# Kernel tuning notes

Hardware: AMD Instinct MI355X
Metric: run time of the kernel (lower is better)

The kernel has to match this reference:

```python
import jax, jax.numpy as jnp
import numpy as np

TAG_THR = 0.1
MIN_HEIGHT = 0.0
PULL_WEIGHT = 1.0
PUSH_WEIGHT = 1.0
EPS = 1e-6


def _bbox_iou(boxes):
    # boxes: [N,4] -> IoU [N,N] (standard, no +1 offset; heights in the loss
    # are also computed without +1)
    x1, y1, x2, y2 = boxes[:, 0], boxes[:, 1], boxes[:, 2], boxes[:, 3]
    area = (x2 - x1) * (y2 - y1)
    iw = jnp.clip(jnp.minimum(x2[:, None], x2[None, :]) - jnp.maximum(x1[:, None], x1[None, :]), 0.0)
    ih = jnp.clip(jnp.minimum(y2[:, None], y2[None, :]) - jnp.maximum(y1[:, None], y1[None, :]), 0.0)
    inter = iw * ih
    union = area[:, None] + area[None, :] - inter
    return inter / jnp.maximum(union, 1e-12)


def _single_image(pred, gt_inds, proposals):
    # pred [N,D], gt_inds [N] int, proposals [N,5]
    N = pred.shape[0]
    heights = proposals[:, 3] - proposals[:, 1]
    valid = (gt_inds >= 0) & (heights > MIN_HEIGHT)
    scores = proposals[:, 4]
    iou = _bbox_iou(proposals[:, :4])  # [N,N]

    def step(state, _):
        alive, tot_pull, tot_push, pull_cnt, push_cnt = state
        active = jnp.sum(alive) >= 2  # pop i; if nothing remains, the torch loop breaks
        # i = highest-scoring remaining proposal (greedy, score-sorted)
        i = jnp.argmax(jnp.where(alive, scores, -jnp.inf))
        rem = alive.at[i].set(False)
        overlap = (iou[i] > 0.0) & rem
        diff = jnp.mean((pred - pred[i]) ** 2, axis=1)  # [N]
        check = diff < TAG_THR
        same = gt_inds == gt_inds[i]
        pull_m = overlap & same & ~check
        push_m = overlap & ~same & check
        pn = jnp.sum(pull_m)
        qn = jnp.sum(push_m)
        pull_l = jnp.sum(jnp.where(pull_m, diff * scores, 0.0)) / jnp.maximum(pn, 1).astype(diff.dtype)
        push_l = jnp.sum(jnp.where(push_m, jnp.exp(-diff) * scores, 0.0)) / jnp.maximum(qn, 1).astype(diff.dtype)
        add_pull = active & (pn > 0)
        add_push = active & (qn > 0)
        tot_pull = tot_pull + jnp.where(add_pull, pull_l, 0.0)
        tot_push = tot_push + jnp.where(add_push, push_l, 0.0)
        pull_cnt = pull_cnt + add_pull.astype(jnp.float32)
        push_cnt = push_cnt + add_push.astype(jnp.float32)
        # suppress everything overlapping i whose tag is already close (diff < thr)
        new_alive = rem & ~(overlap & check)
        alive = jnp.where(active, new_alive, alive)
        return (alive, tot_pull, tot_push, pull_cnt, push_cnt), None

    z = jnp.float32(0.0)
    init = (valid, z, z, z, z)
    (_, tot_pull, tot_push, pull_cnt, push_cnt), _ = jax.lax.scan(step, init, None, length=N)
    pull = tot_pull / (pull_cnt + EPS)
    push = tot_push / (push_cnt + EPS)
    return push, pull


def setup_inputs() -> dict:
    key = jax.random.key(0)
    k1, k2, k3, k4, k5, k6, k7 = jax.random.split(key, 7)
    IMGS, N, D = 4, 2000, 4
    pred = jax.random.normal(k1, (IMGS, N, D), dtype=jnp.float32)
    gt_inds = jax.random.randint(k2, (IMGS, N), 0, 50, dtype=jnp.int32)
    x1 = jax.random.uniform(k3, (IMGS, N), minval=0.0, maxval=800.0)
    y1 = jax.random.uniform(k4, (IMGS, N), minval=0.0, maxval=800.0)
    w = jax.random.uniform(k5, (IMGS, N), minval=8.0, maxval=128.0)
    h = jax.random.uniform(k6, (IMGS, N), minval=8.0, maxval=128.0)
    score = jax.random.uniform(k7, (IMGS, N), minval=0.0, maxval=1.0)
    proposals = jnp.stack([x1, y1, x1 + w, y1 + h, score], axis=-1).astype(jnp.float32)
    gt_bboxes = jax.random.uniform(jax.random.fold_in(key, 9), (IMGS, 20, 4), dtype=jnp.float32)
    return {"pred": pred, "gt_inds": gt_inds, "proposals": proposals, "gt_bboxes": gt_bboxes}


def reference(pred, gt_inds, proposals, gt_bboxes):
    # gt_bboxes is accepted by the torch forward but never used in the loss math.
    push, pull = jax.vmap(_single_image)(pred, gt_inds, proposals)  # per-image scalars
    img_num = pred.shape[0]
    push_loss = jnp.sum(push) / img_num * PUSH_WEIGHT
    pull_loss = jnp.sum(pull) / img_num * PULL_WEIGHT
    return push_loss, pull_loss
```

## Files before the change

### kernel.cpp

```cpp
#include <hip/hip_runtime.h>
#include <stdint.h>

#define BLOCK 256
#define KMAX 8
#define NWAVES (BLOCK / 64)
#define S2 2048
#define NW 32
#define NCH 32
#define SPB 16
#define PB (S2 / SPB)
#define RB (S2 / BLOCK)
#define PCAP 65536
#define LDSP2 4096
#define BCAP 64
#define EFF_INF 0x7FFFFFFF

__device__ inline int rank_of(const unsigned long long* ss, int j) {
    int jw = j >> 6, jb = j & 63;
    int rk = __popcll(ss[jw] & (jb ? (~0ull >> (64 - jb)) : 0ull));
    for (int w = 0; w < jw; ++w) rk += __popcll(ss[w]);
    return rk;
}

__global__ __launch_bounds__(BLOCK) void rankcount_kernel(
    const float* __restrict__ proposals,
    int* __restrict__ partial, int* __restrict__ pcnt, int N, int imgs)
{
    const int bi = blockIdx.x, bj = blockIdx.y, img = blockIdx.z;
    const int t = threadIdx.x;
    if (bi == 0 && bj == 0 && t == 0) pcnt[img] = 0;
    const float* P = proposals + (size_t)img * N * 5;
    __shared__ unsigned sj[BLOCK];
    const int jbase = bj * BLOCK;
    {
        int j = jbase + t;
        sj[t] = (j < N) ? __float_as_uint(P[j*5 + 4]) : 0u;
    }
    __syncthreads();
    const int i = bi * BLOCK + t;
    if (i >= N) return;
    const unsigned my = __float_as_uint(P[i*5 + 4]);
    int p = 0;
    const uint4* s4 = (const uint4*)sj;
#pragma unroll
    for (int q = 0; q < BLOCK/4; ++q) {
        uint4 v = s4[q];
        int jj = jbase + q*4;
        p += (int)((v.x > my) | ((v.x == my) & (jj + 0 < i)));
        p += (int)((v.y > my) | ((v.y == my) & (jj + 1 < i)));
        p += (int)((v.z > my) | ((v.z == my) & (jj + 2 < i)));
        p += (int)((v.w > my) | ((v.w == my) & (jj + 3 < i)));
    }
    partial[((size_t)(img*RB + bj))*S2 + i] = p;
}

__global__ __launch_bounds__(BLOCK) void rankscatter_kernel(
    const float* __restrict__ pred, const int* __restrict__ gt_inds,
    const float* __restrict__ proposals, const int* __restrict__ partial,
    float* __restrict__ soa, int* __restrict__ sgt, int N, int imgs)
{
    const int img = blockIdx.y, t = threadIdx.x;
    const int i = blockIdx.x * BLOCK + t;
    const size_t stride = (size_t)imgs * S2;
    const size_t base   = (size_t)img * S2;

    if (i >= N) {
        if (i < S2) {
#pragma unroll
            for (int a = 0; a < 9; ++a) soa[(size_t)a*stride + base + i] = 0.f;
            sgt[base + i] = -1;
        }
        return;
    }

    const float* P = proposals + (size_t)img * N * 5;
    const float* E = pred      + (size_t)img * N * 4;
    const int*   G = gt_inds   + (size_t)img * N;

    const float p0 = P[i*5+0], p1 = P[i*5+1], p2 = P[i*5+2],
                p3 = P[i*5+3], p4 = P[i*5+4];
    const float q0 = E[i*4+0], q1 = E[i*4+1], q2 = E[i*4+2], q3 = E[i*4+3];
    const int   gg = G[i];

    int p = 0;
#pragma unroll
    for (int b = 0; b < RB; ++b)
        p += partial[((size_t)(img*RB + b))*S2 + i];

    soa[0*stride + base + p] = p0;
    soa[1*stride + base + p] = p1;
    soa[2*stride + base + p] = p2;
    soa[3*stride + base + p] = p3;
    soa[4*stride + base + p] = p4;
    soa[5*stride + base + p] = q0;
    soa[6*stride + base + p] = q1;
    soa[7*stride + base + p] = q2;
    soa[8*stride + base + p] = q3;
    sgt[base + p] = gg;
}

__global__ __launch_bounds__(BLOCK) void suppairs_kernel(
    const float* __restrict__ soa, unsigned* __restrict__ pairs,
    int* __restrict__ pcnt, int N, int imgs)
{
    const int ic = blockIdx.x, jc = blockIdx.y, img = blockIdx.z;
    if (ic < jc) return;
    const int t = threadIdx.x, wave = t >> 6, lane = t & 63;
    const size_t stride = (size_t)imgs * S2, base = (size_t)img * S2;
    __shared__ float si[8][64];
    for (int idx = t; idx < 512; idx += BLOCK) {
        int f = idx >> 6, e = idx & 63;
        int a = (f < 4) ? f : f + 1;
        si[f][e] = soa[(size_t)a*stride + base + ic*64 + e];
    }
    __syncthreads();
    const int j = jc*64 + lane;
    const float jx1 = soa[0*stride+base+j], jy1 = soa[1*stride+base+j];
    const float jx2 = soa[2*stride+base+j], jy2 = soa[3*stride+base+j];
    const float j0  = soa[5*stride+base+j], j1  = soa[6*stride+base+j];
    const float j2  = soa[7*stride+base+j], j3  = soa[8*stride+base+j];
    const bool jin = (j < N);
    unsigned* PL = pairs + (size_t)img * PCAP;
    for (int ii = 0; ii < 16; ++ii) {
        int il = wave*16 + ii;
        int i  = ic*64 + il;
        float bx1 = si[0][il], by1 = si[1][il], bx2 = si[2][il], by2 = si[3][il];
        float f0  = si[4][il], f1  = si[5][il], f2  = si[6][il], f3  = si[7][il];
        bool s = false;
        if (jin && i < N && i > j) {
            float iw = fminf(jx2, bx2) - fmaxf(jx1, bx1);
            float ih = fminf(jy2, by2) - fmaxf(jy1, by1);
            if (iw > 0.f && ih > 0.f) {
                float d0 = j0-f0, d1 = j1-f1, d2 = j2-f2, d3 = j3-f3;
                float diff = 0.25f*(d0*d0 + d1*d1 + d2*d2 + d3*d3);
                s = diff < 0.1f;
            }
        }
        unsigned long long m = __ballot(s);
        if (m) {
            int leader = __ffsll((unsigned long long)m) - 1;
            int basei = 0;
            if (lane == leader) basei = atomicAdd(&pcnt[img], __popcll(m));
            basei = __shfl(basei, leader);
            if (s) {
                int idx = basei + __popcll(m & ((lane == 0) ? 0ull : (~0ull >> (64 - lane))));
                if (idx < PCAP) PL[idx] = ((unsigned)j << 11) | (unsigned)i;
            }
        }
    }
}

__global__ __launch_bounds__(64) void greedy_kernel(
    const unsigned* __restrict__ pairs, const int* __restrict__ pcnt,
    const int* __restrict__ sgt, const float* __restrict__ soa,
    unsigned long long* __restrict__ selw_out, int imgs)
{
    const int img = blockIdx.x, l = threadIdx.x;
    const size_t stride = (size_t)imgs * S2, base = (size_t)img * S2;
    __shared__ unsigned long long slocAll[S2];
    __shared__ unsigned spair[LDSP2];
    __shared__ unsigned bucket[NCH * BCAP];
    __shared__ int bcnt[NCH];
    __shared__ unsigned long long skilled[NW], ssel[NW];

    int P = pcnt[img]; if (P > PCAP) P = PCAP;
    const unsigned* PL = pairs + (size_t)img * PCAP;
    const bool staged = (P <= LDSP2);

    for (int x = l; x < S2; x += 64) slocAll[x] = 0ull;
    if (l < NCH) bcnt[l] = 0;
    if (staged) for (int p = l; p < P; p += 64) spair[p] = PL[p];

    for (int c = 0; c < NCH; ++c) {
        const int j = c*64 + l;
        int g = sgt[base + j];
        float a = soa[1*stride + base + j];
        float b = soa[3*stride + base + j];
        bool invalid = !(g >= 0 && (b - a) > 0.f);
        unsigned long long bb = __ballot(invalid);
        if (l == 0) skilled[c] = bb;
    }
    __syncthreads();

    for (int p = l; p < P; p += 64) {
        unsigned v = staged ? spair[p] : PL[p];
        int lo = v >> 11, hi = v & 2047;
        if ((lo >> 6) == (hi >> 6)) {
            atomicOr(&slocAll[hi], 1ull << (lo & 63));
        } else {
            int idx = atomicAdd(&bcnt[lo >> 6], 1);
            if (idx < BCAP) bucket[(lo >> 6)*BCAP + idx] = v;
        }
    }
    __syncthreads();

    const unsigned long long lowmask = (l == 0) ? 0ull : (~0ull >> (64 - l));

    for (int c = 0; c < NCH; ++c) {
        unsigned long long U = ~skilled[c];
        const unsigned long long loc = slocAll[c*64 + l];
        unsigned long long sel = 0ull;
        while (U) {
            bool inU = (U >> l) & 1ull;
            unsigned long long A = __ballot(inU && ((loc & U & lowmask) == 0ull));
            sel |= A;
            bool kill = inU && !((A >> l) & 1ull) && ((loc & A) != 0ull);
            unsigned long long K = __ballot(kill);
            U &= ~(A | K);
        }
        if (l == 0) ssel[c] = sel;
        if (sel != 0ull) {
            const int bc = bcnt[c];
            if (bc <= BCAP) {
                for (int q = l; q < bc; q += 64) {
                    unsigned v = bucket[c*BCAP + q];
                    int lo = v >> 11, hi = v & 2047;
                    if ((sel >> (lo & 63)) & 1ull)
                        atomicOr(&skilled[hi >> 6], 1ull << (hi & 63));
                }
            } else {
                for (int p = l; p < P; p += 64) {
                    unsigned v = PL[p];
                    int lo = v >> 11, hi = v & 2047;
                    if ((lo >> 6) == c && (hi >> 6) != c &&
                        ((sel >> (lo & 63)) & 1ull))
                        atomicOr(&skilled[hi >> 6], 1ull << (hi & 63));
                }
            }
        }
        __syncthreads();
    }
    if (l < NW) selw_out[(size_t)img*NW + l] = ssel[l];
}

__global__ __launch_bounds__(BLOCK) void effsteps_kernel(
    const unsigned* __restrict__ pairs, const int* __restrict__ pcnt,
    const unsigned long long* __restrict__ selw,
    const int* __restrict__ sgt, const float* __restrict__ soa,
    int* __restrict__ eff, int* __restrict__ nsteps, int imgs)
{
    const int img = blockIdx.x, t = threadIdx.x;
    const int lane = t & 63, wave = t >> 6;
    const size_t stride = (size_t)imgs * S2, base = (size_t)img * S2;
    __shared__ unsigned long long ss[NW];
    __shared__ int sistar[S2];
    __shared__ unsigned hist[S2];
    __shared__ int ints[2*NWAVES];
    __shared__ unsigned wsum[NWAVES];
    __shared__ int bm[NWAVES];
    if (t < NW) ss[t] = selw[(size_t)img*NW + t];
    for (int x = t; x < S2; x += BLOCK) { sistar[x] = EFF_INF; hist[x] = 0u; }
    __syncthreads();

    int P = pcnt[img]; if (P > PCAP) P = PCAP;
    const unsigned* PL = pairs + (size_t)img * PCAP;
    for (int p = t; p < P; p += BLOCK) {
        unsigned v = PL[p];
        int lo = v >> 11, hi = v & 2047;
        if ((ss[lo >> 6] >> (lo & 63)) & 1ull) atomicMin(&sistar[hi], lo);
    }
    __syncthreads();

    int myV = 0, mySc = 0;
#pragma unroll
    for (int k = 0; k < 8; ++k) {
        const int j = k*BLOCK + t;
        int g = sgt[base + j];
        float a = soa[1*stride+base+j], b = soa[3*stride+base+j];
        bool valid = (g >= 0) && ((b - a) > 0.f);
        bool selb  = (ss[j>>6] >> (j & 63)) & 1ull;
        int e;
        if (!valid) e = 0;
        else if (selb) { e = rank_of(ss, j); ++myV; ++mySc; }
        else {
            ++myV;
            int istar = sistar[j];
            if (istar == EFF_INF) e = EFF_INF;
            else { e = rank_of(ss, istar) + 1; atomicAdd(&hist[e - 1], 1u); }
        }
        eff[(size_t)img*S2 + j] = e;
    }
    __syncthreads();

    int v = myV, sc = mySc;
    for (int o = 32; o > 0; o >>= 1) { v += __shfl_down(v, o); sc += __shfl_down(sc, o); }
    if (lane == 0) { ints[wave] = v; ints[NWAVES + wave] = sc; }
    __syncthreads();
    int V = 0, Sc = 0;
    for (int w = 0; w < NWAVES; ++w) { V += ints[w]; Sc += ints[NWAVES + w]; }

    unsigned loc[8]; unsigned s = 0;
#pragma unroll
    for (int k = 0; k < 8; ++k) { s += hist[t*8 + k]; loc[k] = s; }
    unsigned tot = s;
    for (int o = 1; o < 64; o <<= 1) {
        unsigned u = __shfl_up(tot, o);
        if (lane >= o) tot += u;
    }
    if (lane == 63) wsum[wave] = tot;
    __syncthreads();
    unsigned woff = 0;
    for (int w = 0; w < wave; ++w) woff += wsum[w];
    unsigned exclP = woff + tot - s;
    __syncthreads();
#pragma unroll
    for (int k = 0; k < 8; ++k) hist[t*8 + k] = exclP + loc[k];
    __syncthreads();

    int best = EFF_INF;
    for (int r = t; r < Sc; r += BLOCK) {
        unsigned rem = (r == 0) ? 0u : hist[r - 1];
        int alive = V - r - (int)rem;
        if (alive < 2) best = min(best, r);
    }
    for (int o = 32; o > 0; o >>= 1) best = min(best, __shfl_down(best, o));
    if (lane == 0) bm[wave] = best;
    __syncthreads();
    if (t == 0) {
        int b = bm[0];
        for (int w = 1; w < NWAVES; ++w) b = min(b, bm[w]);
        nsteps[img] = min(b, Sc);
    }
}

__global__ __launch_bounds__(BLOCK) void pairs_kernel(
    const float* __restrict__ soa, const int* __restrict__ sgt,
    const int* __restrict__ eff, const unsigned long long* __restrict__ selw,
    const int* __restrict__ nsteps, float* __restrict__ partials, int imgs)
{
    const int ic = blockIdx.x, img = blockIdx.y;
    const int t = threadIdx.x, wave = t >> 6, lane = t & 63;
    const size_t stride = (size_t)imgs * S2, base = (size_t)img * S2;
    __shared__ unsigned long long ss[NW];
    __shared__ float pw[NWAVES][4];
    __shared__ int anyact;
    if (t < NW) ss[t] = selw[(size_t)img*NW + t];
    if (t == 0) anyact = 0;
    __syncthreads();
    const int ns = nsteps[img];

    float bx1[4], by1[4], bx2[4], by2[4], f0[4], f1[4], f2[4], f3[4];
    int bgt[4], rk[4]; bool act[4];
    bool any = false;
#pragma unroll
    for (int u = 0; u < 4; ++u) {
        const int i = ic*SPB + wave*4 + u;
        bool selb = (ss[i>>6] >> (i & 63)) & 1ull;
        int r = rank_of(ss, i);
        rk[u] = r;
        act[u] = selb && (r < ns);
        any |= act[u];
        if (act[u]) {
            bx1[u] = soa[0*stride+base+i]; by1[u] = soa[1*stride+base+i];
            bx2[u] = soa[2*stride+base+i]; by2[u] = soa[3*stride+base+i];
            f0[u]  = soa[5*stride+base+i]; f1[u]  = soa[6*stride+base+i];
            f2[u]  = soa[7*stride+base+i]; f3[u]  = soa[8*stride+base+i];
            bgt[u] = sgt[base + i];
        } else {
            bx1[u]=by1[u]=bx2[u]=by2[u]=0.f; f0[u]=f1[u]=f2[u]=f3[u]=0.f; bgt[u]=-2;
        }
    }
    if (any && lane == 0) anyact = 1;
    __syncthreads();
    if (!anyact) {
        if (t < 4) partials[((size_t)img*PB + ic)*4 + t] = 0.f;
        return;
    }

    float ps[4] = {0,0,0,0}, pn[4] = {0,0,0,0}, qs[4] = {0,0,0,0}, qn[4] = {0,0,0,0};
    for (int jt = 0; jt < NCH; ++jt) {
        const int j = jt*64 + lane;
        const float jx1 = soa[0*stride+base+j], jy1 = soa[1*stride+base+j];
        const float jx2 = soa[2*stride+base+j], jy2 = soa[3*stride+base+j];
        const float jsc = soa[4*stride+base+j];
        const float j0  = soa[5*stride+base+j], j1  = soa[6*stride+base+j];
        const float j2  = soa[7*stride+base+j], j3  = soa[8*stride+base+j];
        const int   jgt = sgt[base + j];
        const int   jef = eff[(size_t)img*S2 + j];
#pragma unroll
        for (int u = 0; u < 4; ++u) {
            if (!act[u]) continue;
            if (rk[u] < jef) {
                float iw = fminf(jx2, bx2[u]) - fmaxf(jx1, bx1[u]);
                float ih = fminf(jy2, by2[u]) - fmaxf(jy1, by1[u]);
                if (iw > 0.f && ih > 0.f) {
                    float d0 = j0 - f0[u], d1 = j1 - f1[u];
                    float d2 = j2 - f2[u], d3 = j3 - f3[u];
                    float diff = 0.25f*(d0*d0 + d1*d1 + d2*d2 + d3*d3);
                    bool check = diff < 0.1f;
                    bool same  = (jgt == bgt[u]);
                    if (same && !check)      { ps[u] += diff * jsc;       pn[u] += 1.f; }
                    else if (!same && check) { qs[u] += expf(-diff)*jsc;  qn[u] += 1.f; }
                }
            }
        }
    }

    float sPull = 0.f, cPull = 0.f, sPush = 0.f, cPush = 0.f;
#pragma unroll
    for (int u = 0; u < 4; ++u) {
        if (!act[u]) continue;
        float a0 = ps[u], a1 = pn[u], a2 = qs[u], a3 = qn[u];
        for (int o = 32; o > 0; o >>= 1) {
            a0 += __shfl_down(a0, o); a1 += __shfl_down(a1, o);
            a2 += __shfl_down(a2, o); a3 += __shfl_down(a3, o);
        }
        if (lane == 0) {
            if (a1 > 0.f) { sPull += a0 / a1; cPull += 1.f; }
            if (a3 > 0.f) { sPush += a2 / a3; cPush += 1.f; }
        }
    }
    if (lane == 0) {
        pw[wave][0] = sPull; pw[wave][1] = cPull;
        pw[wave][2] = sPush; pw[wave][3] = cPush;
    }
    __syncthreads();
    if (t == 0) {
        float a = 0, b = 0, c = 0, d = 0;
        for (int w = 0; w < NWAVES; ++w) {
            a += pw[w][0]; b += pw[w][1]; c += pw[w][2]; d += pw[w][3];
        }
        float* p = partials + ((size_t)img*PB + ic)*4;
        p[0] = a; p[1] = b; p[2] = c; p[3] = d;
    }
}

__global__ __launch_bounds__(BLOCK) void finalize_kernel(
    const float* __restrict__ partials, float* __restrict__ out, int imgs)
{
    const int t = threadIdx.x;
    __shared__ float a[8][4];
    if (t < 32) ((float*)a)[t] = 0.f;
    __syncthreads();
    for (int e = t; e < imgs * PB; e += BLOCK) {
        int img = e / PB;
        const float* p = partials + (size_t)e * 4;
#pragma unroll
        for (int k = 0; k < 4; ++k) {
            float v = p[k];
            if (v != 0.f) atomicAdd(&a[img][k], v);
        }
    }
    __syncthreads();
    if (t == 0) {
        float push = 0.f, pull = 0.f;
        for (int i = 0; i < imgs; ++i) {
            pull += a[i][0] / (a[i][1] + 1e-6f);
            push += a[i][2] / (a[i][3] + 1e-6f);
        }
        out[0] = push / (float)imgs;
        out[1] = pull / (float)imgs;
    }
}

__global__ __launch_bounds__(BLOCK) void tagloss_kernel(
    const float* __restrict__ pred, const int* __restrict__ gt_inds,
    const float* __restrict__ proposals, float* __restrict__ ws, int N)
{
    const int img = blockIdx.x, t = threadIdx.x;
    const int lane = t & 63, wav = t >> 6;
    const float* P = proposals + (size_t)img * N * 5;
    const float* E = pred      + (size_t)img * N * 4;
    const int*   G = gt_inds   + (size_t)img * N;
    float x1[KMAX], y1[KMAX], x2[KMAX], y2[KMAX], sc[KMAX];
    float e0[KMAX], e1[KMAX], e2[KMAX], e3[KMAX];
    int gt[KMAX]; unsigned amask = 0u; int local_alive = 0;
#pragma unroll
    for (int k = 0; k < KMAX; ++k) {
        int j = k * BLOCK + t;
        if (j < N) {
            x1[k]=P[j*5+0]; y1[k]=P[j*5+1]; x2[k]=P[j*5+2]; y2[k]=P[j*5+3]; sc[k]=P[j*5+4];
            e0[k]=E[j*4+0]; e1[k]=E[j*4+1]; e2[k]=E[j*4+2]; e3[k]=E[j*4+3]; gt[k]=G[j];
            if (gt[k] >= 0 && (y2[k]-y1[k]) > 0.0f) { amask |= 1u<<k; local_alive++; }
        } else { x1[k]=y1[k]=x2[k]=y2[k]=0.f; sc[k]=0.f; e0[k]=e1[k]=e2[k]=e3[k]=0.f; gt[k]=-1; }
    }
    __shared__ unsigned long long s_key[NWAVES];
    __shared__ float s_b[9];
    __shared__ float s_part[NWAVES][5];
    int alive_count;
    {
        float v = (float)local_alive;
#pragma unroll
        for (int o = 32; o > 0; o >>= 1) v += __shfl_down(v, o);
        if (lane == 0) s_part[wav][0] = v;
        __syncthreads();
        float tot = 0.f;
        for (int w = 0; w < NWAVES; ++w) tot += s_part[w][0];
        alive_count = (int)tot;
    }
    float tot_pull=0.f, tot_push=0.f, pull_cnt=0.f, push_cnt=0.f;
    while (alive_count >= 2) {
        unsigned long long key = 0ull;
#pragma unroll
        for (int k = 0; k < KMAX; ++k)
            if (amask & (1u<<k)) {
                unsigned long long kk = ((unsigned long long)__float_as_uint(sc[k])<<32)
                                      | (unsigned long long)(0xFFFFFFFFu - (unsigned)(k*BLOCK+t));
                if (kk > key) key = kk;
            }
#pragma unroll
        for (int o = 32; o > 0; o >>= 1) {
            unsigned long long ok = __shfl_down(key, o);
            if (ok > key) key = ok;
        }
// ... 50 lines not shown
        if (T3 > 0.f) { tot_push += T2/T3; push_cnt += 1.f; }
        alive_count -= 1 + (int)T4;
    }
    if (t == 0) {
        ws[img*2+0] = tot_push / (push_cnt + 1e-6f);
        ws[img*2+1] = tot_pull / (pull_cnt + 1e-6f);
    }
}

__global__ void finalize_fb_kernel(const float* __restrict__ ws,
                                   float* __restrict__ out, int imgs)
{
    if (threadIdx.x == 0 && blockIdx.x == 0) {
        float push = 0.f, pull = 0.f;
        for (int k = 0; k < imgs; ++k) { push += ws[2*k]; pull += ws[2*k+1]; }
        out[0] = push / (float)imgs;
        out[1] = pull / (float)imgs;
    }
}

extern "C" void kernel_launch(void* const* d_in, const int* in_sizes, int n_in,
                              void* d_out, int out_size, void* d_ws, size_t ws_size,
                              hipStream_t stream) {
    const float* pred      = (const float*)d_in[0];
    const int*   gt_inds   = (const int*)  d_in[1];
    const float* proposals = (const float*)d_in[2];
    const int imgs = in_sizes[3] / 80;
    const int N    = in_sizes[1] / imgs;

    size_t off = 0;
    auto alloc = [&](size_t b) { size_t o = off; off += (b + 255) & ~(size_t)255; return o; };
    const size_t soa_off  = alloc((size_t)9 * imgs * S2 * 4);
    const size_t sgt_off  = alloc((size_t)imgs * S2 * 4);
    const size_t sel_off  = alloc((size_t)imgs * NW * 8);
    const size_t eff_off  = alloc((size_t)imgs * S2 * 4);
    const size_t nst_off  = alloc((size_t)imgs * 4);
    const size_t par_off  = alloc((size_t)imgs * PB * 16);
    const size_t rnk_off  = alloc((size_t)imgs * RB * S2 * 4);
    const size_t prs_off  = alloc((size_t)imgs * PCAP * 4);
    const size_t pcn_off  = alloc((size_t)imgs * 4);
    const size_t need = off;

    if (N <= S2 && imgs <= 8 && ws_size >= need) {
        char* w = (char*)d_ws;
        float*              soa  = (float*)(w + soa_off);
        int*                sgt  = (int*)(w + sgt_off);
        unsigned long long* sel  = (unsigned long long*)(w + sel_off);
        int*                eff  = (int*)(w + eff_off);
        int*                nst  = (int*)(w + nst_off);
        float*              par  = (float*)(w + par_off);
        int*                rnk  = (int*)(w + rnk_off);
        unsigned*           prs  = (unsigned*)(w + prs_off);
        int*                pcn  = (int*)(w + pcn_off);

        rankcount_kernel<<<dim3(RB, RB, imgs), BLOCK, 0, stream>>>(
            proposals, rnk, pcn, N, imgs);
        rankscatter_kernel<<<dim3(RB, imgs), BLOCK, 0, stream>>>(
            pred, gt_inds, proposals, rnk, soa, sgt, N, imgs);
        suppairs_kernel<<<dim3(NCH, NCH, imgs), BLOCK, 0, stream>>>(
            soa, prs, pcn, N, imgs);
        greedy_kernel<<<imgs, 64, 0, stream>>>(prs, pcn, sgt, soa, sel, imgs);
        effsteps_kernel<<<imgs, BLOCK, 0, stream>>>(prs, pcn, sel, sgt, soa,
                                                    eff, nst, imgs);
        pairs_kernel<<<dim3(PB, imgs), BLOCK, 0, stream>>>(soa, sgt, eff, sel,
                                                           nst, par, imgs);
        finalize_kernel<<<1, BLOCK, 0, stream>>>(par, (float*)d_out, imgs);
    } else {
        float* ws = (float*)d_ws;
        tagloss_kernel<<<imgs, BLOCK, 0, stream>>>(pred, gt_inds, proposals, ws, N);
        finalize_fb_kernel<<<1, 64, 0, stream>>>(ws, (float*)d_out, imgs);
    }
}
```

Before: 152.1 us.

## Fuse seven-stage pipeline into one cooperative persistent kernel with grid syncs

Replaces seven separate kernel launches (rank count, scatter, suppression pairs, greedy, effective steps, pair loss, finalize) with one cooperative kernel of 256 blocks that loops over virtual blocks and separates stages with grid.sync. The aim is to remove per-launch overhead and inter-kernel gaps. The greedy and effsteps stages now run only on a few blocks of a 256-thread grid, and the rest of the grid sits idle at the barriers. Grid syncs add their own cost, and single-image stages limit parallelism.

```diff
diff --git a/kernel.cpp b/kernel.cpp
--- a/kernel.cpp
+++ b/kernel.cpp
@@ -1,7 +1,11 @@
 #include <hip/hip_runtime.h>
+#include <hip/hip_cooperative_groups.h>
 #include <stdint.h>
 
+namespace cg = cooperative_groups;
+
 #define BLOCK 256
+#define GRIDN 256
 #define KMAX 8
 #define NWAVES (BLOCK / 64)
 #define S2 2048
@@ -10,446 +14,452 @@
 #define SPB 16
 #define PB (S2 / SPB)
 #define RB (S2 / BLOCK)
+#define NTRI (NCH*(NCH+1)/2)
 #define PCAP 65536
 #define LDSP2 4096
 #define BCAP 64
 #define EFF_INF 0x7FFFFFFF
 
-__device__ inline int rank_of(const unsigned long long* ss, int j) {
-    int jw = j >> 6, jb = j & 63;
-    int rk = __popcll(ss[jw] & (jb ? (~0ull >> (64 - jb)) : 0ull));
-    for (int w = 0; w < jw; ++w) rk += __popcll(ss[w]);
-    return rk;
-}
-
-__global__ __launch_bounds__(BLOCK) void rankcount_kernel(
+struct SmallD {
+    int bcnt[NCH];
+    unsigned long long skilled[NW];
+    unsigned long long ssel[NW];
+    unsigned long long svalid[NW];
+    int pfx[NW + 1];
+    float pw[NWAVES][4];
+    unsigned wsum[NWAVES];
+    int bm[NWAVES];
+    int sV;
+    int anyact;
+};
+
+__global__ __launch_bounds__(BLOCK) void mega_kernel(
+    const float* __restrict__ pred, const int* __restrict__ gt_inds,
     const float* __restrict__ proposals,
-    int* __restrict__ partial, int* __restrict__ pcnt, int N, int imgs)
+    float* __restrict__ soa, int* __restrict__ sgt, int* __restrict__ rnk,
+    unsigned* __restrict__ prs, int* __restrict__ pcn,
+    unsigned long long* __restrict__ selw, int* __restrict__ eff,
+    int* __restrict__ nst, float* __restrict__ par, float* __restrict__ out,
+    int N, int imgs)
 {
-    const int bi = blockIdx.x, bj = blockIdx.y, img = blockIdx.z;
-    const int t = threadIdx.x;
-    if (bi == 0 && bj == 0 && t == 0) pcnt[img] = 0;
-    const float* P = proposals + (size_t)img * N * 5;
-    __shared__ unsigned sj[BLOCK];
-    const int jbase = bj * BLOCK;
+    cg::grid_group grid = cg::this_grid();
+    const int blk = blockIdx.x, t = threadIdx.x;
+    const int lane = t & 63, wave = t >> 6;
+    const size_t stride = (size_t)imgs * S2;
+
+    __shared__ __align__(16) char SM[43008];
+    char* A = SM;
+    unsigned* spair = (unsigned*)(SM + 16384);
+    unsigned* bucket = (unsigned*)(SM + 32768);
+    SmallD* D = (SmallD*)(SM + 40960);
+
     {
-        int j = jbase + t;
-        sj[t] = (j < N) ? __float_as_uint(P[j*5 + 4]) : 0u;
-    }
-    __syncthreads();
-    const int i = bi * BLOCK + t;
-    if (i >= N) return;
-    const unsigned my = __float_as_uint(P[i*5 + 4]);
-    int p = 0;
-    const uint4* s4 = (const uint4*)sj;
-#pragma unroll
-    for (int q = 0; q < BLOCK/4; ++q) {
-        uint4 v = s4[q];
-        int jj = jbase + q*4;
-        p += (int)((v.x > my) | ((v.x == my) & (jj + 0 < i)));
-        p += (int)((v.y > my) | ((v.y == my) & (jj + 1 < i)));
-        p += (int)((v.z > my) | ((v.z == my) & (jj + 2 < i)));
-        p += (int)((v.w > my) | ((v.w == my) & (jj + 3 < i)));
-    }
-    partial[((size_t)(img*RB + bj))*S2 + i] = p;
-}
-
-__global__ __launch_bounds__(BLOCK) void rankscatter_kernel(
-    const float* __restrict__ pred, const int* __restrict__ gt_inds,
-    const float* __restrict__ proposals, const int* __restrict__ partial,
-    float* __restrict__ soa, int* __restrict__ sgt, int N, int imgs)
-{
-    const int img = blockIdx.y, t = threadIdx.x;
-    const int i = blockIdx.x * BLOCK + t;
-    const size_t stride = (size_t)imgs * S2;
-    const size_t base   = (size_t)img * S2;
-
-    if (i >= N) {
-        if (i < S2) {
-#pragma unroll
-            for (int a = 0; a < 9; ++a) soa[(size_t)a*stride + base + i] = 0.f;
-            sgt[base + i] = -1;
-        }
-        return;
-    }
-
-    const float* P = proposals + (size_t)img * N * 5;
-    const float* E = pred      + (size_t)img * N * 4;
-    const int*   G = gt_inds   + (size_t)img * N;
-
-    const float p0 = P[i*5+0], p1 = P[i*5+1], p2 = P[i*5+2],
-                p3 = P[i*5+3], p4 = P[i*5+4];
-    const float q0 = E[i*4+0], q1 = E[i*4+1], q2 = E[i*4+2], q3 = E[i*4+3];
-    const int   gg = G[i];
-
-    int p = 0;
-#pragma unroll
-    for (int b = 0; b < RB; ++b)
-        p += partial[((size_t)(img*RB + b))*S2 + i];
-
-    soa[0*stride + base + p] = p0;
-    soa[1*stride + base + p] = p1;
-    soa[2*stride + base + p] = p2;
-    soa[3*stride + base + p] = p3;
-    soa[4*stride + base + p] = p4;
-    soa[5*stride + base + p] = q0;
-    soa[6*stride + base + p] = q1;
-    soa[7*stride + base + p] = q2;
-    soa[8*stride + base + p] = q3;
-    sgt[base + p] = gg;
-}
-
-__global__ __launch_bounds__(BLOCK) void suppairs_kernel(
-    const float* __restrict__ soa, unsigned* __restrict__ pairs,
-    int* __restrict__ pcnt, int N, int imgs)
-{
-    const int ic = blockIdx.x, jc = blockIdx.y, img = blockIdx.z;
-    if (ic < jc) return;
-    const int t = threadIdx.x, wave = t >> 6, lane = t & 63;
-    const size_t stride = (size_t)imgs * S2, base = (size_t)img * S2;
-    __shared__ float si[8][64];
-    for (int idx = t; idx < 512; idx += BLOCK) {
-        int f = idx >> 6, e = idx & 63;
-        int a = (f < 4) ? f : f + 1;
-        si[f][e] = soa[(size_t)a*stride + base + ic*64 + e];
-    }
-    __syncthreads();
-    const int j = jc*64 + lane;
-    const float jx1 = soa[0*stride+base+j], jy1 = soa[1*stride+base+j];
-    const float jx2 = soa[2*stride+base+j], jy2 = soa[3*stride+base+j];
-    const float j0  = soa[5*stride+base+j], j1  = soa[6*stride+base+j];
-    const float j2  = soa[7*stride+base+j], j3  = soa[8*stride+base+j];
-    const bool jin = (j < N);
-    unsigned* PL = pairs + (size_t)img * PCAP;
-    for (int ii = 0; ii < 16; ++ii) {
-        int il = wave*16 + ii;
-        int i  = ic*64 + il;
-        float bx1 = si[0][il], by1 = si[1][il], bx2 = si[2][il], by2 = si[3][il];
-        float f0  = si[4][il], f1  = si[5][il], f2  = si[6][il], f3  = si[7][il];
-        bool s = false;
-        if (jin && i < N && i > j) {
-            float iw = fminf(jx2, bx2) - fmaxf(jx1, bx1);
-            float ih = fminf(jy2, by2) - fmaxf(jy1, by1);
-            if (iw > 0.f && ih > 0.f) {
-                float d0 = j0-f0, d1 = j1-f1, d2 = j2-f2, d3 = j3-f3;
-                float diff = 0.25f*(d0*d0 + d1*d1 + d2*d2 + d3*d3);
-                s = diff < 0.1f;
-            }
-        }
-        unsigned long long m = __ballot(s);
-        if (m) {
-            int leader = __ffsll((unsigned long long)m) - 1;
-            int basei = 0;
-            if (lane == leader) basei = atomicAdd(&pcnt[img], __popcll(m));
-            basei = __shfl(basei, leader);
-            if (s) {
-                int idx = basei + __popcll(m & ((lane == 0) ? 0ull : (~0ull >> (64 - lane))));
-                if (idx < PCAP) PL[idx] = ((unsigned)j << 11) | (unsigned)i;
-            }
-        }
-    }
-}
-
-__global__ __launch_bounds__(64) void greedy_kernel(
-    const unsigned* __restrict__ pairs, const int* __restrict__ pcnt,
-    const int* __restrict__ sgt, const float* __restrict__ soa,
-    unsigned long long* __restrict__ selw_out, int imgs)
-{
-    const int img = blockIdx.x, l = threadIdx.x;
-    const size_t stride = (size_t)imgs * S2, base = (size_t)img * S2;
-    __shared__ unsigned long long slocAll[S2];
-    __shared__ unsigned spair[LDSP2];
-    __shared__ unsigned bucket[NCH * BCAP];
-    __shared__ int bcnt[NCH];
-    __shared__ unsigned long long skilled[NW], ssel[NW];
-
-    int P = pcnt[img]; if (P > PCAP) P = PCAP;
-    const unsigned* PL = pairs + (size_t)img * PCAP;
-    const bool staged = (P <= LDSP2);
-
-    for (int x = l; x < S2; x += 64) slocAll[x] = 0ull;
-    if (l < NCH) bcnt[l] = 0;
-    if (staged) for (int p = l; p < P; p += 64) spair[p] = PL[p];
-
-    for (int c = 0; c < NCH; ++c) {
-        const int j = c*64 + l;
-        int g = sgt[base + j];
-        float a = soa[1*stride + base + j];
-        float b = soa[3*stride + base + j];
-        bool invalid = !(g >= 0 && (b - a) > 0.f);
-        unsigned long long bb = __ballot(invalid);
-        if (l == 0) skilled[c] = bb;
-    }
-    __syncthreads();
-
-    for (int p = l; p < P; p += 64) {
-        unsigned v = staged ? spair[p] : PL[p];
-        int lo = v >> 11, hi = v & 2047;
-        if ((lo >> 6) == (hi >> 6)) {
-            atomicOr(&slocAll[hi], 1ull << (lo & 63));
-        } else {
-            int idx = atomicAdd(&bcnt[lo >> 6], 1);
-            if (idx < BCAP) bucket[(lo >> 6)*BCAP + idx] = v;
-        }
-    }
-    __syncthreads();
-
-    const unsigned long long lowmask = (l == 0) ? 0ull : (~0ull >> (64 - l));
-
-    for (int c = 0; c < NCH; ++c) {
-        unsigned long long U = ~skilled[c];
-        const unsigned long long loc = slocAll[c*64 + l];
-        unsigned long long sel = 0ull;
-        while (U) {
-            bool inU = (U >> l) & 1ull;
-            unsigned long long A = __ballot(inU && ((loc & U & lowmask) == 0ull));
-            sel |= A;
-            bool kill = inU && !((A >> l) & 1ull) && ((loc & A) != 0ull);
-            unsigned long long K = __ballot(kill);
-            U &= ~(A | K);
-        }
-        if (l == 0) ssel[c] = sel;
-        if (sel != 0ull) {
-            const int bc = bcnt[c];
-            if (bc <= BCAP) {
-                for (int q = l; q < bc; q += 64) {
-                    unsigned v = bucket[c*BCAP + q];
-                    int lo = v >> 11, hi = v & 2047;
-                    if ((sel >> (lo & 63)) & 1ull)
-                        atomicOr(&skilled[hi >> 6], 1ull << (hi & 63));
-                }
+        unsigned* sj = (unsigned*)A;
+        if (blk == 0 && t < imgs) pcn[t] = 0;
+        const int T0 = RB * RB * imgs;
+        for (int vb = blk; vb < T0; vb += GRIDN) {
+            const int img = vb / (RB * RB);
+            const int rem = vb % (RB * RB);
+            const int bi = rem / RB, bj = rem % RB;
+            const float* P = proposals + (size_t)img * N * 5;
+            __syncthreads();
+            {
+                int j = bj * BLOCK + t;
+                sj[t] = (j < N) ? __float_as_uint(P[j*5 + 4]) : 0u;
+            }
+            __syncthreads();
+            const int i = bi * BLOCK + t;
+            if (i < N) {
+                const unsigned my = __float_as_uint(P[i*5 + 4]);
+                int p = 0;
+                const uint4* s4 = (const uint4*)sj;
+#pragma unroll
+                for (int q = 0; q < BLOCK/4; ++q) {
+                    uint4 v = s4[q];
+                    int jj = bj * BLOCK + q*4;
+                    p += (int)((v.x > my) | ((v.x == my) & (jj + 0 < i)));
+                    p += (int)((v.y > my) | ((v.y == my) & (jj + 1 < i)));
+                    p += (int)((v.z > my) | ((v.z == my) & (jj + 2 < i)));
+                    p += (int)((v.w > my) | ((v.w == my) & (jj + 3 < i)));
+                }
+                rnk[((size_t)(img*RB + bj))*S2 + i] = p;
+            }
+        }
+    }
+    grid.sync();
+
+    {
+        const int T1 = RB * imgs;
+        for (int vb = blk; vb < T1; vb += GRIDN) {
+            const int img = vb / RB, bi = vb % RB;
+            const int i = bi * BLOCK + t;
+            const size_t base = (size_t)img * S2;
+            if (i >= N) {
+                if (i < S2) {
+#pragma unroll
+                    for (int a = 0; a < 9; ++a) soa[(size_t)a*stride + base + i] = 0.f;
+                    sgt[base + i] = -1;
+                }
+                continue;
+            }
+            const float* P = proposals + (size_t)img * N * 5;
+            const float* E = pred      + (size_t)img * N * 4;
+            const int*   G = gt_inds   + (size_t)img * N;
+            const float p0 = P[i*5+0], p1 = P[i*5+1], p2 = P[i*5+2],
+                        p3 = P[i*5+3], p4 = P[i*5+4];
+            const float q0 = E[i*4+0], q1 = E[i*4+1], q2 = E[i*4+2], q3 = E[i*4+3];
+            const int   gv = G[i];
+            int p = 0;
+#pragma unroll
+            for (int b = 0; b < RB; ++b)
+                p += rnk[((size_t)(img*RB + b))*S2 + i];
+            soa[0*stride + base + p] = p0;
+            soa[1*stride + base + p] = p1;
+            soa[2*stride + base + p] = p2;
+            soa[3*stride + base + p] = p3;
+            soa[4*stride + base + p] = p4;
+            soa[5*stride + base + p] = q0;
+            soa[6*stride + base + p] = q1;
+            soa[7*stride + base + p] = q2;
+            soa[8*stride + base + p] = q3;
+            sgt[base + p] = gv;
+        }
+    }
+    grid.sync();
+
+    {
+        float (*si)[64] = (float(*)[64])A;
+        const int T2 = NTRI * imgs;
+        for (int vb = blk; vb < T2; vb += GRIDN) {
+            const int img = vb / NTRI;
+            const int tri = vb % NTRI;
+            int ic = 0;
+            while ((ic + 1)*(ic + 2)/2 <= tri) ++ic;
+            const int jc = tri - ic*(ic + 1)/2;
+            const size_t base = (size_t)img * S2;
+            __syncthreads();
+            for (int idx = t; idx < 512; idx += BLOCK) {
+                int f = idx >> 6, e = idx & 63;
+                int a = (f < 4) ? f : f + 1;
+                si[f][e] = soa[(size_t)a*stride + base + ic*64 + e];
+            }
+            __syncthreads();
+            const int j = jc*64 + lane;
+            const float jx1 = soa[0*stride+base+j], jy1 = soa[1*stride+base+j];
+            const float jx2 = soa[2*stride+base+j], jy2 = soa[3*stride+base+j];
+            const float j0  = soa[5*stride+base+j], j1  = soa[6*stride+base+j];
+            const float j2  = soa[7*stride+base+j], j3  = soa[8*stride+base+j];
+            const bool jin = (j < N);
+            unsigned* PL = prs + (size_t)img * PCAP;
+            for (int ii = 0; ii < 16; ++ii) {
+                int il = wave*16 + ii;
+                int i  = ic*64 + il;
+                bool s = false;
+                if (jin && i < N && i > j) {
+                    float iw = fminf(jx2, si[2][il]) - fmaxf(jx1, si[0][il]);
+                    float ih = fminf(jy2, si[3][il]) - fmaxf(jy1, si[1][il]);
+                    if (iw > 0.f && ih > 0.f) {
+                        float d0 = j0-si[4][il], d1 = j1-si[5][il];
+                        float d2 = j2-si[6][il], d3 = j3-si[7][il];
+                        float diff = 0.25f*(d0*d0 + d1*d1 + d2*d2 + d3*d3);
+                        s = diff < 0.1f;
+                    }
+                }
+                unsigned long long m = __ballot(s);
+                if (m) {
+                    int leader = __ffsll((unsigned long long)m) - 1;
+                    int basei = 0;
+                    if (lane == leader) basei = atomicAdd(&pcn[img], __popcll(m));
+                    basei = __shfl(basei, leader);
+                    if (s) {
+                        int idx = basei + __popcll(m & ((lane == 0) ? 0ull : (~0ull >> (64 - lane))));
+                        if (idx < PCAP) PL[idx] = ((unsigned)j << 11) | (unsigned)i;
+                    }
+                }
+            }
+        }
+    }
+    grid.sync();
+
+    if (blk < imgs) {
+        const int img = blk;
+        const size_t base = (size_t)img * S2;
+        unsigned long long* slocAll = (unsigned long long*)A;
+
+        int P = pcn[img]; if (P > PCAP) P = PCAP;
+        const unsigned* PL = prs + (size_t)img * PCAP;
+        const bool staged = (P <= LDSP2);
+
+        for (int x = t; x < S2; x += BLOCK) slocAll[x] = 0ull;
+        if (t < NCH) D->bcnt[t] = 0;
+        if (t == 0) D->sV = 0;
+        __syncthreads();
+        if (staged) for (int p = t; p < P; p += BLOCK) spair[p] = PL[p];
+        for (int g = wave; g < NCH; g += NWAVES) {
+            int j = g*64 + lane;
+            int gv = sgt[base + j];
+            float a = soa[1*stride + base + j];
+            float b = soa[3*stride + base + j];
+            bool invalid = !(gv >= 0 && (b - a) > 0.f);
+            unsigned long long bb = __ballot(invalid);
+            if (lane == 0) {
+                D->skilled[g] = bb;
+                D->svalid[g] = ~bb;
+                atomicAdd(&D->sV, 64 - __popcll(bb));
+            }
+        }
+        __syncthreads();
+        for (int p = t; p < P; p += BLOCK) {
+            unsigned v = staged ? spair[p] : PL[p];
+            int lo = v >> 11, hi = v & 2047;
+            if ((lo >> 6) == (hi >> 6)) {
+                atomicOr(&slocAll[hi], 1ull << (lo & 63));
             } else {
-                for (int p = l; p < P; p += 64) {
-                    unsigned v = PL[p];
-                    int lo = v >> 11, hi = v & 2047;
-                    if ((lo >> 6) == c && (hi >> 6) != c &&
-                        ((sel >> (lo & 63)) & 1ull))
-                        atomicOr(&skilled[hi >> 6], 1ull << (hi & 63));
-                }
-            }
-        }
-        __syncthreads();
-    }
-    if (l < NW) selw_out[(size_t)img*NW + l] = ssel[l];
-}
-
-__global__ __launch_bounds__(BLOCK) void effsteps_kernel(
-    const unsigned* __restrict__ pairs, const int* __restrict__ pcnt,
-    const unsigned long long* __restrict__ selw,
-    const int* __restrict__ sgt, const float* __restrict__ soa,
-    int* __restrict__ eff, int* __restrict__ nsteps, int imgs)
-{
-    const int img = blockIdx.x, t = threadIdx.x;
-    const int lane = t & 63, wave = t >> 6;
-    const size_t stride = (size_t)imgs * S2, base = (size_t)img * S2;
-    __shared__ unsigned long long ss[NW];
-    __shared__ int sistar[S2];
-    __shared__ unsigned hist[S2];
-    __shared__ int ints[2*NWAVES];
-    __shared__ unsigned wsum[NWAVES];
-    __shared__ int bm[NWAVES];
-    if (t < NW) ss[t] = selw[(size_t)img*NW + t];
-    for (int x = t; x < S2; x += BLOCK) { sistar[x] = EFF_INF; hist[x] = 0u; }
-    __syncthreads();
-
-    int P = pcnt[img]; if (P > PCAP) P = PCAP;
-    const unsigned* PL = pairs + (size_t)img * PCAP;
-    for (int p = t; p < P; p += BLOCK) {
-        unsigned v = PL[p];
-        int lo = v >> 11, hi = v & 2047;
-        if ((ss[lo >> 6] >> (lo & 63)) & 1ull) atomicMin(&sistar[hi], lo);
-    }
-    __syncthreads();
-
-    int myV = 0, mySc = 0;
-#pragma unroll
-    for (int k = 0; k < 8; ++k) {
-        const int j = k*BLOCK + t;
-        int g = sgt[base + j];
-        float a = soa[1*stride+base+j], b = soa[3*stride+base+j];
-        bool valid = (g >= 0) && ((b - a) > 0.f);
-        bool selb  = (ss[j>>6] >> (j & 63)) & 1ull;
-        int e;
-        if (!valid) e = 0;
-        else if (selb) { e = rank_of(ss, j); ++myV; ++mySc; }
-        else {
-            ++myV;
-            int istar = sistar[j];
-            if (istar == EFF_INF) e = EFF_INF;
-            else { e = rank_of(ss, istar) + 1; atomicAdd(&hist[e - 1], 1u); }
-        }
-        eff[(size_t)img*S2 + j] = e;
-    }
-    __syncthreads();
-
-    int v = myV, sc = mySc;
-    for (int o = 32; o > 0; o >>= 1) { v += __shfl_down(v, o); sc += __shfl_down(sc, o); }
-    if (lane == 0) { ints[wave] = v; ints[NWAVES + wave] = sc; }
-    __syncthreads();
-    int V = 0, Sc = 0;
-    for (int w = 0; w < NWAVES; ++w) { V += ints[w]; Sc += ints[NWAVES + w]; }
-
-    unsigned loc[8]; unsigned s = 0;
-#pragma unroll
-    for (int k = 0; k < 8; ++k) { s += hist[t*8 + k]; loc[k] = s; }
-    unsigned tot = s;
-    for (int o = 1; o < 64; o <<= 1) {
-        unsigned u = __shfl_up(tot, o);
-        if (lane >= o) tot += u;
-    }
-    if (lane == 63) wsum[wave] = tot;
-    __syncthreads();
-    unsigned woff = 0;
-    for (int w = 0; w < wave; ++w) woff += wsum[w];
-    unsigned exclP = woff + tot - s;
-    __syncthreads();
-#pragma unroll
-    for (int k = 0; k < 8; ++k) hist[t*8 + k] = exclP + loc[k];
-    __syncthreads();
-
-    int best = EFF_INF;
-    for (int r = t; r < Sc; r += BLOCK) {
-        unsigned rem = (r == 0) ? 0u : hist[r - 1];
-        int alive = V - r - (int)rem;
-        if (alive < 2) best = min(best, r);
-    }
-    for (int o = 32; o > 0; o >>= 1) best = min(best, __shfl_down(best, o));
-    if (lane == 0) bm[wave] = best;
-    __syncthreads();
-    if (t == 0) {
-        int b = bm[0];
-        for (int w = 1; w < NWAVES; ++w) b = min(b, bm[w]);
-        nsteps[img] = min(b, Sc);
-    }
-}
-
-__global__ __launch_bounds__(BLOCK) void pairs_kernel(
-    const float* __restrict__ soa, const int* __restrict__ sgt,
-    const int* __restrict__ eff, const unsigned long long* __restrict__ selw,
-    const int* __restrict__ nsteps, float* __restrict__ partials, int imgs)
-{
-    const int ic = blockIdx.x, img = blockIdx.y;
-    const int t = threadIdx.x, wave = t >> 6, lane = t & 63;
-    const size_t stride = (size_t)imgs * S2, base = (size_t)img * S2;
-    __shared__ unsigned long long ss[NW];
-    __shared__ float pw[NWAVES][4];
-    __shared__ int anyact;
-    if (t < NW) ss[t] = selw[(size_t)img*NW + t];
-    if (t == 0) anyact = 0;
-    __syncthreads();
-    const int ns = nsteps[img];
-
-    float bx1[4], by1[4], bx2[4], by2[4], f0[4], f1[4], f2[4], f3[4];
-    int bgt[4], rk[4]; bool act[4];
-    bool any = false;
-#pragma unroll
-    for (int u = 0; u < 4; ++u) {
-        const int i = ic*SPB + wave*4 + u;
-        bool selb = (ss[i>>6] >> (i & 63)) & 1ull;
-        int r = rank_of(ss, i);
-        rk[u] = r;
-        act[u] = selb && (r < ns);
-        any |= act[u];
-        if (act[u]) {
-            bx1[u] = soa[0*stride+base+i]; by1[u] = soa[1*stride+base+i];
-            bx2[u] = soa[2*stride+base+i]; by2[u] = soa[3*stride+base+i];
-            f0[u]  = soa[5*stride+base+i]; f1[u]  = soa[6*stride+base+i];
-            f2[u]  = soa[7*stride+base+i]; f3[u]  = soa[8*stride+base+i];
-            bgt[u] = sgt[base + i];
-        } else {
-            bx1[u]=by1[u]=bx2[u]=by2[u]=0.f; f0[u]=f1[u]=f2[u]=f3[u]=0.f; bgt[u]=-2;
-        }
-    }
-    if (any && lane == 0) anyact = 1;
-    __syncthreads();
-    if (!anyact) {
-        if (t < 4) partials[((size_t)img*PB + ic)*4 + t] = 0.f;
-        return;
-    }
-
-    float ps[4] = {0,0,0,0}, pn[4] = {0,0,0,0}, qs[4] = {0,0,0,0}, qn[4] = {0,0,0,0};
-    for (int jt = 0; jt < NCH; ++jt) {
-        const int j = jt*64 + lane;
-        const float jx1 = soa[0*stride+base+j], jy1 = soa[1*stride+base+j];
-        const float jx2 = soa[2*stride+base+j], jy2 = soa[3*stride+base+j];
-        const float jsc = soa[4*stride+base+j];
-        const float j0  = soa[5*stride+base+j], j1  = soa[6*stride+base+j];
-        const float j2  = soa[7*stride+base+j], j3  = soa[8*stride+base+j];
-        const int   jgt = sgt[base + j];
-        const int   jef = eff[(size_t)img*S2 + j];
-#pragma unroll
-        for (int u = 0; u < 4; ++u) {
-            if (!act[u]) continue;
-            if (rk[u] < jef) {
-                float iw = fminf(jx2, bx2[u]) - fmaxf(jx1, bx1[u]);
-                float ih = fminf(jy2, by2[u]) - fmaxf(jy1, by1[u]);
-                if (iw > 0.f && ih > 0.f) {
-                    float d0 = j0 - f0[u], d1 = j1 - f1[u];
-                    float d2 = j2 - f2[u], d3 = j3 - f3[u];
-                    float diff = 0.25f*(d0*d0 + d1*d1 + d2*d2 + d3*d3);
-                    bool check = diff < 0.1f;
-                    bool same  = (jgt == bgt[u]);
-                    if (same && !check)      { ps[u] += diff * jsc;       pn[u] += 1.f; }
-                    else if (!same && check) { qs[u] += expf(-diff)*jsc;  qn[u] += 1.f; }
-                }
-            }
-        }
-    }
-
-    float sPull = 0.f, cPull = 0.f, sPush = 0.f, cPush = 0.f;
-#pragma unroll
-    for (int u = 0; u < 4; ++u) {
-        if (!act[u]) continue;
-        float a0 = ps[u], a1 = pn[u], a2 = qs[u], a3 = qn[u];
-        for (int o = 32; o > 0; o >>= 1) {
-            a0 += __shfl_down(a0, o); a1 += __shfl_down(a1, o);
-            a2 += __shfl_down(a2, o); a3 += __shfl_down(a3, o);
-        }
-        if (lane == 0) {
-            if (a1 > 0.f) { sPull += a0 / a1; cPull += 1.f; }
-            if (a3 > 0.f) { sPush += a2 / a3; cPush += 1.f; }
-        }
-    }
-    if (lane == 0) {
-        pw[wave][0] = sPull; pw[wave][1] = cPull;
-        pw[wave][2] = sPush; pw[wave][3] = cPush;
-    }
-    __syncthreads();
-    if (t == 0) {
-        float a = 0, b = 0, c = 0, d = 0;
-        for (int w = 0; w < NWAVES; ++w) {
-            a += pw[w][0]; b += pw[w][1]; c += pw[w][2]; d += pw[w][3];
-        }
-        float* p = partials + ((size_t)img*PB + ic)*4;
-        p[0] = a; p[1] = b; p[2] = c; p[3] = d;
-    }
-}
-
-__global__ __launch_bounds__(BLOCK) void finalize_kernel(
-    const float* __restrict__ partials, float* __restrict__ out, int imgs)
-{
-    const int t = threadIdx.x;
-    __shared__ float a[8][4];
-    if (t < 32) ((float*)a)[t] = 0.f;
-    __syncthreads();
-    for (int e = t; e < imgs * PB; e += BLOCK) {
-        int img = e / PB;
-        const float* p = partials + (size_t)e * 4;
-#pragma unroll
-        for (int k = 0; k < 4; ++k) {
-            float v = p[k];
-            if (v != 0.f) atomicAdd(&a[img][k], v);
-        }
-    }
-    __syncthreads();
-    if (t == 0) {
-        float push = 0.f, pull = 0.f;
-        for (int i = 0; i < imgs; ++i) {
-            pull += a[i][0] / (a[i][1] + 1e-6f);
-            push += a[i][2] / (a[i][3] + 1e-6f);
-        }
-        out[0] = push / (float)imgs;
-        out[1] = pull / (float)imgs;
+                int idx = atomicAdd(&D->bcnt[lo >> 6], 1);
+                if (idx < BCAP) bucket[(lo >> 6)*BCAP + idx] = v;
+            }
+        }
+        __syncthreads();
+
+        if (wave == 0) {
+            const unsigned long long lowmask = (lane == 0) ? 0ull : (~0ull >> (64 - lane));
+            for (int c = 0; c < NCH; ++c) {
+                unsigned long long U = ~D->skilled[c];
+                const unsigned long long loc = slocAll[c*64 + lane];
+                unsigned long long sel = 0ull;
+                while (U) {
+                    bool inU = (U >> lane) & 1ull;
+                    unsigned long long Am = __ballot(inU && ((loc & U & lowmask) == 0ull));
+                    sel |= Am;
+                    bool kill = inU && !((Am >> lane) & 1ull) && ((loc & Am) != 0ull);
+                    unsigned long long K = __ballot(kill);
+                    U &= ~(Am | K);
+                }
+                if (lane == 0) D->ssel[c] = sel;
+                if (sel != 0ull) {
+                    const int bc = D->bcnt[c];
+                    if (bc <= BCAP) {
+                        for (int q = lane; q < bc; q += 64) {
+                            unsigned v = bucket[c*BCAP + q];
+                            int lo = v >> 11, hi = v & 2047;
+                            if ((sel >> (lo & 63)) & 1ull)
+                                atomicOr(&D->skilled[hi >> 6], 1ull << (hi & 63));
+                        }
+                    } else {
+                        for (int p = lane; p < P; p += 64) {
+                            unsigned v = PL[p];
+                            int lo = v >> 11, hi = v & 2047;
+                            if ((lo >> 6) == c && (hi >> 6) != c &&
+                                ((sel >> (lo & 63)) & 1ull))
+                                atomicOr(&D->skilled[hi >> 6], 1ull << (hi & 63));
+                        }
+                    }
+                }
+            }
+        }
+        __syncthreads();
+        if (t < NW) selw[(size_t)img*NW + t] = D->ssel[t];
+
+        int* sistar = (int*)A;
+        unsigned* hist = (unsigned*)(A + 8192);
+        for (int x = t; x < S2; x += BLOCK) { sistar[x] = EFF_INF; hist[x] = 0u; }
+        if (t == 0) {
+            int s = 0;
+            for (int w = 0; w < NW; ++w) { D->pfx[w] = s; s += __popcll(D->ssel[w]); }
+            D->pfx[NW] = s;
+        }
+        __syncthreads();
+        for (int p = t; p < P; p += BLOCK) {
+            unsigned v = staged ? spair[p] : PL[p];
+            int lo = v >> 11, hi = v & 2047;
+            if ((D->ssel[lo >> 6] >> (lo & 63)) & 1ull) atomicMin(&sistar[hi], lo);
+        }
+        __syncthreads();
+#pragma unroll
+        for (int k = 0; k < 8; ++k) {
+            const int j = k*BLOCK + t;
+            const int jw = j >> 6, jb = j & 63;
+            bool valid = (D->svalid[jw] >> jb) & 1ull;
+            bool selb  = (D->ssel[jw] >> jb) & 1ull;
+            int e;
+            if (!valid) e = 0;
+            else if (selb)
+                e = D->pfx[jw] + __popcll(D->ssel[jw] & (jb ? (~0ull >> (64 - jb)) : 0ull));
+            else {
+                int is = sistar[j];
+                if (is == EFF_INF) e = EFF_INF;
+                else {
+                    int iw_ = is >> 6, ib = is & 63;
+                    e = D->pfx[iw_] + __popcll(D->ssel[iw_] & (ib ? (~0ull >> (64 - ib)) : 0ull)) + 1;
+                    atomicAdd(&hist[e - 1], 1u);
+                }
+            }
+            eff[(size_t)img*S2 + j] = e;
+        }
+        __syncthreads();
+
+        const int V = D->sV, Sc = D->pfx[NW];
+        unsigned loc8[8]; unsigned s = 0;
+#pragma unroll
+        for (int k = 0; k < 8; ++k) { s += hist[t*8 + k]; loc8[k] = s; }
+        unsigned tot = s;
+        for (int o = 1; o < 64; o <<= 1) {
+            unsigned u = __shfl_up(tot, o);
+            if (lane >= o) tot += u;
+        }
+        if (lane == 63) D->wsum[wave] = tot;
+        __syncthreads();
+        unsigned woff = 0;
+        for (int w = 0; w < wave; ++w) woff += D->wsum[w];
+        unsigned exclP = woff + tot - s;
+        __syncthreads();
+#pragma unroll
+        for (int k = 0; k < 8; ++k) hist[t*8 + k] = exclP + loc8[k];
+        __syncthreads();
+        int best = EFF_INF;
+        for (int r = t; r < Sc; r += BLOCK) {
+            unsigned rem = (r == 0) ? 0u : hist[r - 1];
+            int alive = V - r - (int)rem;
+            if (alive < 2) best = min(best, r);
+        }
+        for (int o = 32; o > 0; o >>= 1) best = min(best, __shfl_down(best, o));
+        if (lane == 0) D->bm[wave] = best;
+        __syncthreads();
+        if (t == 0) {
+            int b = D->bm[0];
+            for (int w = 1; w < NWAVES; ++w) b = min(b, D->bm[w]);
+            nst[img] = min(b, Sc);
+        }
+    }
+    grid.sync();
+
+    {
+        const int T4 = PB * imgs;
+        for (int vb = blk; vb < T4; vb += GRIDN) {
+            const int img = vb / PB, ic = vb % PB;
+            const size_t base = (size_t)img * S2;
+            __syncthreads();
+            if (t < NW) D->ssel[t] = selw[(size_t)img*NW + t];
+            if (t == 0) D->anyact = 0;
+            __syncthreads();
+            if (t == 0) {
+                int s = 0;
+                for (int w = 0; w < NW; ++w) { D->pfx[w] = s; s += __popcll(D->ssel[w]); }
+                D->pfx[NW] = s;
+            }
+            __syncthreads();
+            const int ns = nst[img];
+            float bx1[4], by1[4], bx2[4], by2[4], f0[4], f1[4], f2[4], f3[4];
+            int bgt[4], rk[4]; bool act[4];
+            bool any = false;
+#pragma unroll
+            for (int u = 0; u < 4; ++u) {
+                const int i = ic*SPB + wave*4 + u;
+                const int iw_ = i >> 6, ib = i & 63;
+                bool selb = (D->ssel[iw_] >> ib) & 1ull;
+                int r = D->pfx[iw_] + __popcll(D->ssel[iw_] & (ib ? (~0ull >> (64 - ib)) : 0ull));
+                rk[u] = r;
+                act[u] = selb && (r < ns);
+                any |= act[u];
+                if (act[u]) {
+                    bx1[u] = soa[0*stride+base+i]; by1[u] = soa[1*stride+base+i];
+                    bx2[u] = soa[2*stride+base+i]; by2[u] = soa[3*stride+base+i];
+                    f0[u]  = soa[5*stride+base+i]; f1[u]  = soa[6*stride+base+i];
+                    f2[u]  = soa[7*stride+base+i]; f3[u]  = soa[8*stride+base+i];
+                    bgt[u] = sgt[base + i];
+                } else {
+                    bx1[u]=by1[u]=bx2[u]=by2[u]=0.f; f0[u]=f1[u]=f2[u]=f3[u]=0.f; bgt[u]=-2;
+                }
+            }
+            if (any && lane == 0) D->anyact = 1;
+            __syncthreads();
+
+            float sPull = 0.f, cPull = 0.f, sPush = 0.f, cPush = 0.f;
+            if (D->anyact) {
+                float ps[4] = {0,0,0,0}, pn[4] = {0,0,0,0};
+                float qs[4] = {0,0,0,0}, qn[4] = {0,0,0,0};
+                for (int jt = 0; jt < NCH; ++jt) {
+                    const int j = jt*64 + lane;
+                    const float jx1 = soa[0*stride+base+j], jy1 = soa[1*stride+base+j];
+                    const float jx2 = soa[2*stride+base+j], jy2 = soa[3*stride+base+j];
+                    const float jsc = soa[4*stride+base+j];
+                    const float j0  = soa[5*stride+base+j], j1  = soa[6*stride+base+j];
+                    const float j2  = soa[7*stride+base+j], j3  = soa[8*stride+base+j];
+                    const int   jgt = sgt[base + j];
+                    const int   jef = eff[(size_t)img*S2 + j];
+#pragma unroll
+                    for (int u = 0; u < 4; ++u) {
+                        if (!act[u]) continue;
+                        if (rk[u] < jef) {
+                            float iw = fminf(jx2, bx2[u]) - fmaxf(jx1, bx1[u]);
+                            float ih = fminf(jy2, by2[u]) - fmaxf(jy1, by1[u]);
+                            if (iw > 0.f && ih > 0.f) {
+                                float d0 = j0 - f0[u], d1 = j1 - f1[u];
+                                float d2 = j2 - f2[u], d3 = j3 - f3[u];
+                                float diff = 0.25f*(d0*d0 + d1*d1 + d2*d2 + d3*d3);
+                                bool check = diff < 0.1f;
+                                bool same  = (jgt == bgt[u]);
+                                if (same && !check)      { ps[u] += diff * jsc;       pn[u] += 1.f; }
+                                else if (!same && check) { qs[u] += expf(-diff)*jsc;  qn[u] += 1.f; }
+                            }
+                        }
+                    }
+                }
+#pragma unroll
+                for (int u = 0; u < 4; ++u) {
+                    if (!act[u]) continue;
+                    float a0 = ps[u], a1 = pn[u], a2 = qs[u], a3 = qn[u];
+                    for (int o = 32; o > 0; o >>= 1) {
+                        a0 += __shfl_down(a0, o); a1 += __shfl_down(a1, o);
+                        a2 += __shfl_down(a2, o); a3 += __shfl_down(a3, o);
+                    }
+                    if (lane == 0) {
+                        if (a1 > 0.f) { sPull += a0 / a1; cPull += 1.f; }
+                        if (a3 > 0.f) { sPush += a2 / a3; cPush += 1.f; }
+                    }
+                }
+            }
+            if (lane == 0) {
+                D->pw[wave][0] = sPull; D->pw[wave][1] = cPull;
+                D->pw[wave][2] = sPush; D->pw[wave][3] = cPush;
+            }
+            __syncthreads();
+            if (t == 0) {
+                float a = 0, b = 0, c = 0, d = 0;
+                for (int w = 0; w < NWAVES; ++w) {
+                    a += D->pw[w][0]; b += D->pw[w][1];
+                    c += D->pw[w][2]; d += D->pw[w][3];
+                }
+                float* p = par + (size_t)vb * 4;
+                p[0] = a; p[1] = b; p[2] = c; p[3] = d;
+            }
+        }
+    }
+    grid.sync();
+
+    if (blk == 0) {
+        float (*a)[4] = (float(*)[4])A;
+        if (t < 32) ((float*)a)[t] = 0.f;
+        __syncthreads();
+        for (int e = t; e < imgs * PB; e += BLOCK) {
+            int img = e / PB;
+            const float* p = par + (size_t)e * 4;
+#pragma unroll
+            for (int k = 0; k < 4; ++k) {
+                float v = p[k];
+                if (v != 0.f) atomicAdd(&a[img][k], v);
+            }
+        }
+        __syncthreads();
+        if (t == 0) {
+            float push = 0.f, pull = 0.f;
+            for (int i = 0; i < imgs; ++i) {
+                pull += a[i][0] / (a[i][1] + 1e-6f);
+                push += a[i][2] / (a[i][3] + 1e-6f);
+            }
+            out[0] = push / (float)imgs;
+            out[1] = pull / (float)imgs;
+        }
     }
 }
 
@@ -606,19 +616,17 @@
         int*                rnk  = (int*)(w + rnk_off);
         unsigned*           prs  = (unsigned*)(w + prs_off);
         int*                pcn  = (int*)(w + pcn_off);
-
-        rankcount_kernel<<<dim3(RB, RB, imgs), BLOCK, 0, stream>>>(
-            proposals, rnk, pcn, N, imgs);
-        rankscatter_kernel<<<dim3(RB, imgs), BLOCK, 0, stream>>>(
-            pred, gt_inds, proposals, rnk, soa, sgt, N, imgs);
-        suppairs_kernel<<<dim3(NCH, NCH, imgs), BLOCK, 0, stream>>>(
-            soa, prs, pcn, N, imgs);
-        greedy_kernel<<<imgs, 64, 0, stream>>>(prs, pcn, sgt, soa, sel, imgs);
-        effsteps_kernel<<<imgs, BLOCK, 0, stream>>>(prs, pcn, sel, sgt, soa,
-                                                    eff, nst, imgs);
-        pairs_kernel<<<dim3(PB, imgs), BLOCK, 0, stream>>>(soa, sgt, eff, sel,
-                                                           nst, par, imgs);
-        finalize_kernel<<<1, BLOCK, 0, stream>>>(par, (float*)d_out, imgs);
+        float*              outp = (float*)d_out;
+        int nN = N, nimgs = imgs;
+
+        void* args[] = {
+            (void*)&pred, (void*)&gt_inds, (void*)&proposals,
+            (void*)&soa, (void*)&sgt, (void*)&rnk, (void*)&prs, (void*)&pcn,
+            (void*)&sel, (void*)&eff, (void*)&nst, (void*)&par, (void*)&outp,
+            (void*)&nN, (void*)&nimgs
+        };
+        hipLaunchCooperativeKernel((const void*)mega_kernel,
+                                   dim3(GRIDN), dim3(BLOCK), args, 0, stream);
     } else {
         float* ws = (float*)d_ws;
         tagloss_kernel<<<imgs, BLOCK, 0, stream>>>(pred, gt_inds, proposals, ws, N);
```

Measured after the change: 307.1 us. +101.9%, slower.
